# Performance work log

Hardware: AMD Instinct MI355X
Metric: run time of the kernel (lower is better)

## Reference

```python
import jax, jax.numpy as jnp
import numpy as np

TOKENS, D_IN, D_OUT = 16384, 2048, 2048


def setup_inputs() -> dict:
    key = jax.random.key(0)
    k1, k2, k3 = jax.random.split(key, 3)
    x = jax.random.normal(k1, (TOKENS, D_IN), dtype=jnp.float32)
    # int8 quantized weight, stored transposed as [in_features, out_features]
    weight = jax.random.randint(k2, (D_IN, D_OUT), -128, 128).astype(jnp.int8)
    # per-output-channel dequant scale, shape [1, out_features]
    scale = (jax.random.uniform(k3, (1, D_OUT), dtype=jnp.float32) * 0.01 + 1e-4)
    return {"x": x, "scale": scale, "weight": weight}


def reference(x, scale, weight):
    # x: [N, in], weight: int8 [in, out] (pre-transposed), scale: [1, out]
    tokens = x.shape[:-1]
    xf = x.reshape(-1, x.shape[-1])
    # cast int8 weight to activation dtype, dense matmul, per-channel scale
    y = jnp.matmul(xf, weight.astype(x.dtype)) * scale
    # bias path is dead in the original (`if self.bias:` on a tensor); omitted
    return y.reshape(tokens + (weight.shape[-1],))
```

## Files before the change

### kernel.cpp

```cpp
#include <hip/hip_runtime.h>
#include <cstdint>


#define M_TOK 16384
#define K_DIM 2048
#define N_DIM 2048

typedef _Float16 f16;
typedef f16 f16x4 __attribute__((ext_vector_type(4)));
typedef f16 f16x8 __attribute__((ext_vector_type(8)));
typedef float f32x4 __attribute__((ext_vector_type(4)));

__global__ void convert_x_kernel(const float* __restrict__ x, f16* __restrict__ xh) {
  const int n4 = (M_TOK * K_DIM) / 4;
  const int stride = gridDim.x * blockDim.x;
  for (int i = blockIdx.x * blockDim.x + threadIdx.x; i < n4; i += stride) {
    float4 v = ((const float4*)x)[i];
    f16x4 h;
    h[0] = (f16)v.x; h[1] = (f16)v.y; h[2] = (f16)v.z; h[3] = (f16)v.w;
    ((f16x4*)xh)[i] = h;
  }
}

__global__ void convert_w_kernel(const int* __restrict__ w, f16* __restrict__ wt) {
  __shared__ f16 tile[64][68];
  const int tid = threadIdx.x;
  const int nb = blockIdx.x * 64;
  const int kb = blockIdx.y * 64;
  const int cq = tid & 15;
  const int rr = tid >> 4;

#pragma unroll
  for (int g = 0; g < 4; ++g) {
    int krow = g * 16 + rr;
    const int* p = w + (size_t)(kb + krow) * N_DIM + nb + cq * 4;
    int4 v = *(const int4*)p;
    tile[cq * 4 + 0][krow] = (f16)(float)v.x;
    tile[cq * 4 + 1][krow] = (f16)(float)v.y;
    tile[cq * 4 + 2][krow] = (f16)(float)v.z;
    tile[cq * 4 + 3][krow] = (f16)(float)v.w;
  }
  __syncthreads();
#pragma unroll
  for (int g = 0; g < 4; ++g) {
    int nrow = g * 16 + rr;
    f16x4 o;
#pragma unroll
    for (int j = 0; j < 4; ++j)
      o[j] = tile[nrow][cq * 4 + j];
    *(f16x4*)(wt + (size_t)(nb + nrow) * K_DIM + kb + cq * 4) = o;
  }
}

__device__ __forceinline__ void async_load16(const void* g, void* l) {
  __builtin_amdgcn_global_load_lds((__attribute__((address_space(1))) void*)g,
                                   (__attribute__((address_space(3))) void*)l,
                                   16, 0, 0);
}

#define FENCE() asm volatile("" ::: "memory")
#define BAR()   do { FENCE(); __builtin_amdgcn_s_barrier(); FENCE(); } while (0)
#define LGKM0() asm volatile("s_waitcnt lgkmcnt(0)" ::: "memory")
#define VMCNT_6() asm volatile("s_waitcnt vmcnt(6)" ::: "memory")
#define VMCNT_0() asm volatile("s_waitcnt vmcnt(0)" ::: "memory")

__global__ __launch_bounds__(512, 2) void gemm_8ph(
    const f16* __restrict__ xh, const f16* __restrict__ wt,
    const float* __restrict__ scale, float* __restrict__ out) {
  __shared__ __align__(16) f16 sm[2][4][128 * 64];

  const int tid  = threadIdx.x;
  const int wid  = tid >> 6;
  const int lane = tid & 63;
  const int wr = wid >> 2;
  const int wc = wid & 3;
  const int fr = lane & 15;
  const int kq = lane >> 4;

  const int bid = blockIdx.x;
  const int swz = (bid & 7) * 64 + (bid >> 3);
  const int n0 = (swz & 7) * 256;
  const int m0 = (swz >> 3) * 256;

  const int l8   = lane >> 3;
  const int slot = (lane & 7) ^ l8;
  const int c0   = wid * 2;
  const int row0 = c0 * 8 + l8;
  const int row1 = row0 + 8;

  const f16* gA0 = xh + (size_t)(m0 + (row0 >> 6) * 128 + (row0 & 63)) * K_DIM + slot * 8;
  const f16* gA1 = xh + (size_t)(m0 + (row1 >> 6) * 128 + (row1 & 63)) * K_DIM + slot * 8;
  const f16* gB0 = wt + (size_t)(n0 + (row0 >> 5) * 64 + (row0 & 31)) * K_DIM + slot * 8;
  const f16* gB1 = wt + (size_t)(n0 + (row1 >> 5) * 64 + (row1 & 31)) * K_DIM + slot * 8;

#define STAGE_A(buf, mh, koff) do { \
    async_load16(gA0 + (mh) * 64 * K_DIM + (koff), &sm[buf][mh][c0 * 512]); \
    async_load16(gA1 + (mh) * 64 * K_DIM + (koff), &sm[buf][mh][c0 * 512 + 512]); \
  } while (0)
#define STAGE_B(buf, nh, koff) do { \
    async_load16(gB0 + (nh) * 32 * K_DIM + (koff), &sm[buf][2 + (nh)][c0 * 512]); \
    async_load16(gB1 + (nh) * 32 * K_DIM + (koff), &sm[buf][2 + (nh)][c0 * 512 + 512]); \
  } while (0)

  const int kx0 = (kq * 8) ^ ((fr & 7) * 8);
  const int kx1 = (32 + kq * 8) ^ ((fr & 7) * 8);

  f16x8 a[4][2];
  f16x8 b[2][2][2];
  f32x4 acc[8][4] = {};

#define LDA(buf, mh) do { \
    const f16* base_ = &sm[buf][mh][(wr * 64 + fr) * 64]; \
    _Pragma("unroll") for (int mi_ = 0; mi_ < 4; ++mi_) { \
      a[mi_][0] = *(const f16x8*)(base_ + mi_ * 1024 + kx0); \
      a[mi_][1] = *(const f16x8*)(base_ + mi_ * 1024 + kx1); \
    } } while (0)
#define LDB(buf, nh) do { \
    const f16* base_ = &sm[buf][2 + (nh)][(wc * 32 + fr) * 64]; \
    _Pragma("unroll") for (int ni_ = 0; ni_ < 2; ++ni_) { \
      b[nh][ni_][0] = *(const f16x8*)(base_ + ni_ * 1024 + kx0); \
      b[nh][ni_][1] = *(const f16x8*)(base_ + ni_ * 1024 + kx1); \
    } } while (0)
#define MMA(mh, nh) do { \
    __builtin_amdgcn_s_setprio(1); \
    _Pragma("unroll") for (int mi_ = 0; mi_ < 4; ++mi_) \
    _Pragma("unroll") for (int ni_ = 0; ni_ < 2; ++ni_) { \
      acc[(mh)*4+mi_][(nh)*2+ni_] = __builtin_amdgcn_mfma_f32_16x16x32_f16( \
          a[mi_][0], b[nh][ni_][0], acc[(mh)*4+mi_][(nh)*2+ni_], 0, 0, 0); \
      acc[(mh)*4+mi_][(nh)*2+ni_] = __builtin_amdgcn_mfma_f32_16x16x32_f16( \
          a[mi_][1], b[nh][ni_][1], acc[(mh)*4+mi_][(nh)*2+ni_], 0, 0, 0); \
    } \
    __builtin_amdgcn_s_setprio(0); } while (0)

  STAGE_A(0, 0, 0); STAGE_B(0, 0, 0); STAGE_B(0, 1, 0); STAGE_A(0, 1, 0);
  STAGE_A(1, 0, 64); STAGE_B(1, 0, 64); STAGE_B(1, 1, 64);
  VMCNT_6();
  BAR();

#pragma unroll 1
  for (int i = 0; i < 15; ++i) {
    const int k0 = i * 128;
    LDA(0, 0); LDB(0, 0); STAGE_A(1, 1, k0 + 64);
    BAR(); LGKM0(); MMA(0, 0); BAR();
    LDB(0, 1); STAGE_A(0, 0, k0 + 128);
    BAR(); LGKM0(); MMA(0, 1); BAR();
    LDA(0, 1); STAGE_B(0, 0, k0 + 128);
    BAR(); LGKM0(); MMA(1, 0); BAR();
    STAGE_B(0, 1, k0 + 128);
    BAR(); MMA(1, 1); VMCNT_6(); BAR();
    LDA(1, 0); LDB(1, 0); STAGE_A(0, 1, k0 + 128);
    BAR(); LGKM0(); MMA(0, 0); BAR();
    LDB(1, 1); STAGE_A(1, 0, k0 + 192);
    BAR(); LGKM0(); MMA(0, 1); BAR();
    LDA(1, 1); STAGE_B(1, 0, k0 + 192);
    BAR(); LGKM0(); MMA(1, 0); BAR();
    STAGE_B(1, 1, k0 + 192);
    BAR(); MMA(1, 1); VMCNT_6(); BAR();
  }

  {
    const int k0 = 15 * 128;
    LDA(0, 0); LDB(0, 0); STAGE_A(1, 1, k0 + 64);
    BAR(); LGKM0(); MMA(0, 0); BAR();
    LDB(0, 1);
    BAR(); LGKM0(); MMA(0, 1); BAR();
    LDA(0, 1);
    BAR(); LGKM0(); MMA(1, 0); BAR();
    BAR(); MMA(1, 1); VMCNT_0(); BAR();
    LDA(1, 0); LDB(1, 0);
    BAR(); LGKM0(); MMA(0, 0); BAR();
    LDB(1, 1);
    BAR(); LGKM0(); MMA(0, 1); BAR();
    LDA(1, 1);
    BAR(); LGKM0(); MMA(1, 0); BAR();
    MMA(1, 1);
  }

#pragma unroll
  for (int ni = 0; ni < 4; ++ni) {
    const int col = n0 + wc * 64 + (ni >> 1) * 32 + (ni & 1) * 16 + fr;
    const float s = scale[col];
#pragma unroll
    for (int mi = 0; mi < 8; ++mi) {
      const int rbase = m0 + wr * 128 + (mi >> 2) * 64 + (mi & 3) * 16 + kq * 4;
      f32x4 v = acc[mi][ni];
#pragma unroll
      for (int r = 0; r < 4; ++r)
        out[(size_t)(rbase + r) * N_DIM + col] = v[r] * s;
    }
  }
#undef STAGE_A
#undef STAGE_B
#undef LDA
#undef LDB
#undef MMA
}

extern "C" void kernel_launch(void* const* d_in, const int* in_sizes, int n_in,
                              void* d_out, int out_size, void* d_ws, size_t ws_size,
                              hipStream_t stream) {
  const float* x     = (const float*)d_in[0];
  const float* scale = (const float*)d_in[1];
  const int* w       = (const int*)d_in[2];
  float* out         = (float*)d_out;

  char* ws = (char*)d_ws;
  f16* xh = (f16*)ws;
  f16* wt = (f16*)(ws + (size_t)M_TOK * K_DIM * 2);

  convert_x_kernel<<<8192, 256, 0, stream>>>(x, xh);
  convert_w_kernel<<<dim3(N_DIM / 64, K_DIM / 64), 256, 0, stream>>>(w, wt);
  gemm_8ph<<<dim3((N_DIM / 256) * (M_TOK / 256)), 512, 0, stream>>>(xh, wt, scale, out);
}
```

Measured before the change: 351.2 us.

## Double-buffer MFMA register fragments so LDS reads overlap the previous phase's MFMAs

Splits the A/B register fragments into two sets and reissues the 8-phase schedule so each phase's LDS reads load into the buffer that the next MFMA group will use, while the current MFMAs run on the other. Explicit lgkmcnt(0) waits are dropped and the compiler is left to insert them. The global prefetch order and vmcnt thresholds are also reshuffled. This raises VGPR pressure under launch_bounds(512,2) and relies on the compiler placing correct LDS waits, which risks spills or serialization.

```diff
diff --git a/kernel.cpp b/kernel.cpp
--- a/kernel.cpp
+++ b/kernel.cpp
@@ -60,9 +60,7 @@
 
 #define FENCE() asm volatile("" ::: "memory")
 #define BAR()   do { FENCE(); __builtin_amdgcn_s_barrier(); FENCE(); } while (0)
-#define LGKM0() asm volatile("s_waitcnt lgkmcnt(0)" ::: "memory")
-#define VMCNT_6() asm volatile("s_waitcnt vmcnt(6)" ::: "memory")
-#define VMCNT_0() asm volatile("s_waitcnt vmcnt(0)" ::: "memory")
+#define VMCNT(n) asm volatile("s_waitcnt vmcnt(" #n ")" ::: "memory")
 
 __global__ __launch_bounds__(512, 2) void gemm_8ph(
     const f16* __restrict__ xh, const f16* __restrict__ wt,
@@ -105,75 +103,74 @@
   const int kx0 = (kq * 8) ^ ((fr & 7) * 8);
   const int kx1 = (32 + kq * 8) ^ ((fr & 7) * 8);
 
-  f16x8 a[4][2];
-  f16x8 b[2][2][2];
+  f16x8 a0[4][2], a1[4][2];
+  f16x8 b0[2][2], b1[2][2];
   f32x4 acc[8][4] = {};
 
-#define LDA(buf, mh) do { \
+#define LDA_(dst, buf, mh) do { \
     const f16* base_ = &sm[buf][mh][(wr * 64 + fr) * 64]; \
     _Pragma("unroll") for (int mi_ = 0; mi_ < 4; ++mi_) { \
-      a[mi_][0] = *(const f16x8*)(base_ + mi_ * 1024 + kx0); \
-      a[mi_][1] = *(const f16x8*)(base_ + mi_ * 1024 + kx1); \
+      dst[mi_][0] = *(const f16x8*)(base_ + mi_ * 1024 + kx0); \
+      dst[mi_][1] = *(const f16x8*)(base_ + mi_ * 1024 + kx1); \
     } } while (0)
-#define LDB(buf, nh) do { \
+#define LDB_(dst, buf, nh) do { \
     const f16* base_ = &sm[buf][2 + (nh)][(wc * 32 + fr) * 64]; \
     _Pragma("unroll") for (int ni_ = 0; ni_ < 2; ++ni_) { \
-      b[nh][ni_][0] = *(const f16x8*)(base_ + ni_ * 1024 + kx0); \
-      b[nh][ni_][1] = *(const f16x8*)(base_ + ni_ * 1024 + kx1); \
+      dst[ni_][0] = *(const f16x8*)(base_ + ni_ * 1024 + kx0); \
+      dst[ni_][1] = *(const f16x8*)(base_ + ni_ * 1024 + kx1); \
     } } while (0)
-#define MMA(mh, nh) do { \
+#define MMA(A, B, mh, nh) do { \
     __builtin_amdgcn_s_setprio(1); \
     _Pragma("unroll") for (int mi_ = 0; mi_ < 4; ++mi_) \
     _Pragma("unroll") for (int ni_ = 0; ni_ < 2; ++ni_) { \
       acc[(mh)*4+mi_][(nh)*2+ni_] = __builtin_amdgcn_mfma_f32_16x16x32_f16( \
-          a[mi_][0], b[nh][ni_][0], acc[(mh)*4+mi_][(nh)*2+ni_], 0, 0, 0); \
+          A[mi_][0], B[ni_][0], acc[(mh)*4+mi_][(nh)*2+ni_], 0, 0, 0); \
       acc[(mh)*4+mi_][(nh)*2+ni_] = __builtin_amdgcn_mfma_f32_16x16x32_f16( \
-          a[mi_][1], b[nh][ni_][1], acc[(mh)*4+mi_][(nh)*2+ni_], 0, 0, 0); \
+          A[mi_][1], B[ni_][1], acc[(mh)*4+mi_][(nh)*2+ni_], 0, 0, 0); \
     } \
     __builtin_amdgcn_s_setprio(0); } while (0)
 
-  STAGE_A(0, 0, 0); STAGE_B(0, 0, 0); STAGE_B(0, 1, 0); STAGE_A(0, 1, 0);
-  STAGE_A(1, 0, 64); STAGE_B(1, 0, 64); STAGE_B(1, 1, 64);
-  VMCNT_6();
+  STAGE_A(0, 0, 0);  STAGE_B(0, 0, 0);  STAGE_B(0, 1, 0);  STAGE_A(0, 1, 0);
+  STAGE_A(1, 0, 64); STAGE_B(1, 0, 64); STAGE_B(1, 1, 64); STAGE_A(1, 1, 64);
+  VMCNT(8);
   BAR();
+  LDA_(a0, 0, 0); LDB_(b0, 0, 0);
 
 #pragma unroll 1
   for (int i = 0; i < 15; ++i) {
     const int k0 = i * 128;
-    LDA(0, 0); LDB(0, 0); STAGE_A(1, 1, k0 + 64);
-    BAR(); LGKM0(); MMA(0, 0); BAR();
-    LDB(0, 1); STAGE_A(0, 0, k0 + 128);
-    BAR(); LGKM0(); MMA(0, 1); BAR();
-    LDA(0, 1); STAGE_B(0, 0, k0 + 128);
-    BAR(); LGKM0(); MMA(1, 0); BAR();
-    STAGE_B(0, 1, k0 + 128);
-    BAR(); MMA(1, 1); VMCNT_6(); BAR();
-    LDA(1, 0); LDB(1, 0); STAGE_A(0, 1, k0 + 128);
-    BAR(); LGKM0(); MMA(0, 0); BAR();
-    LDB(1, 1); STAGE_A(1, 0, k0 + 192);
-    BAR(); LGKM0(); MMA(0, 1); BAR();
-    LDA(1, 1); STAGE_B(1, 0, k0 + 192);
-    BAR(); LGKM0(); MMA(1, 0); BAR();
-    STAGE_B(1, 1, k0 + 192);
-    BAR(); MMA(1, 1); VMCNT_6(); BAR();
+    LDB_(b1, 0, 1);
+    BAR(); MMA(a0, b0, 0, 0); BAR();
+    LDA_(a1, 0, 1); STAGE_A(0, 0, k0 + 128);
+    BAR(); MMA(a0, b1, 0, 1); BAR();
+    STAGE_B(0, 0, k0 + 128);
+    BAR(); MMA(a1, b0, 1, 0); VMCNT(4); BAR();
+    LDA_(a0, 1, 0); LDB_(b0, 1, 0); STAGE_B(0, 1, k0 + 128);
+    BAR(); MMA(a1, b1, 1, 1); BAR();
+    LDB_(b1, 1, 1); STAGE_A(0, 1, k0 + 128);
+    BAR(); MMA(a0, b0, 0, 0); BAR();
+    LDA_(a1, 1, 1); STAGE_A(1, 0, k0 + 192);
+    BAR(); MMA(a0, b1, 0, 1); BAR();
+    STAGE_B(1, 0, k0 + 192);
+    BAR(); MMA(a1, b0, 1, 0); VMCNT(8); BAR();
+    LDA_(a0, 0, 0); LDB_(b0, 0, 0); STAGE_B(1, 1, k0 + 192); STAGE_A(1, 1, k0 + 192);
+    BAR(); MMA(a1, b1, 1, 1); VMCNT(8); BAR();
   }
 
   {
-    const int k0 = 15 * 128;
-    LDA(0, 0); LDB(0, 0); STAGE_A(1, 1, k0 + 64);
-    BAR(); LGKM0(); MMA(0, 0); BAR();
-    LDB(0, 1);
-    BAR(); LGKM0(); MMA(0, 1); BAR();
-    LDA(0, 1);
-    BAR(); LGKM0(); MMA(1, 0); BAR();
-    BAR(); MMA(1, 1); VMCNT_0(); BAR();
-    LDA(1, 0); LDB(1, 0);
-    BAR(); LGKM0(); MMA(0, 0); BAR();
-    LDB(1, 1);
-    BAR(); LGKM0(); MMA(0, 1); BAR();
-    LDA(1, 1);
-    BAR(); LGKM0(); MMA(1, 0); BAR();
-    MMA(1, 1);
+    LDB_(b1, 0, 1);
+    BAR(); MMA(a0, b0, 0, 0); BAR();
+    LDA_(a1, 0, 1);
+    BAR(); MMA(a0, b1, 0, 1); BAR();
+    BAR(); MMA(a1, b0, 1, 0); VMCNT(0); BAR();
+    LDA_(a0, 1, 0); LDB_(b0, 1, 0);
+    BAR(); MMA(a1, b1, 1, 1); BAR();
+    LDB_(b1, 1, 1);
+    BAR(); MMA(a0, b0, 0, 0); BAR();
+    LDA_(a1, 1, 1);
+    BAR(); MMA(a0, b1, 0, 1); BAR();
+    BAR(); MMA(a1, b0, 1, 0); BAR();
+    MMA(a1, b1, 1, 1);
   }
 
 #pragma unroll
@@ -191,8 +188,8 @@
   }
 #undef STAGE_A
 #undef STAGE_B
-#undef LDA
-#undef LDB
+#undef LDA_
+#undef LDB_
 #undef MMA
 }
 
```

Result: slower. 411.4 us (+17.1%).
